# Kernel optimization log

Measured on AMD Instinct MI355X. Metric: run time of the kernel, lower is better.

Reference implementation:

```python
import jax, jax.numpy as jnp
import numpy as np

TOP_K = 2
EPS = 1e-10


def setup_inputs() -> dict:
    key = jax.random.key(0)
    k1, k2, k3, k4 = jax.random.split(key, 4)
    B, S, H, E = 4, 2048, 1024, 8
    tokens = jax.random.normal(k1, (B, S, H), dtype=jnp.float32)
    router_w = jax.random.normal(k2, (E, H), dtype=jnp.float32) * (1.0 / np.sqrt(H))
    router_b = jax.random.normal(k3, (E,), dtype=jnp.float32) * 0.01
    expert_weights = jax.random.normal(k4, (E, H, H), dtype=jnp.float32) * (1.0 / np.sqrt(H))
    return {"tokens": tokens, "router_w": router_w, "router_b": router_b,
            "expert_weights": expert_weights}


def reference(tokens, router_w, router_b, expert_weights):
    B, S, H = tokens.shape
    E = expert_weights.shape[0]
    # Router (torch Linear: x @ W^T + b)
    logits = jnp.einsum('bsh,eh->bse', tokens, router_w) + router_b  # [B,S,E]
    probs = jax.nn.softmax(logits, axis=-1)
    top_p, top_i = jax.lax.top_k(probs, TOP_K)            # [B,S,K]
    w = top_p / (jnp.sum(top_p, axis=-1, keepdims=True) + EPS)  # normalized weights

    x = tokens.reshape(-1, H)                              # [N,H]
    idx = top_i.reshape(-1, TOP_K)                         # [N,K]
    wf = w.reshape(-1, TOP_K)                              # [N,K]

    # Expert GEMM: compute all experts then gather selected (dense, vectorized
    # equivalent of the sort/pad/grouped-GEMM dispatch; padded rows with
    # original_indices==-1 never contribute to the output).
    y_all = jnp.einsum('nh,ehd->ned', x, expert_weights)   # [N,E,H]
    y_k = jnp.take_along_axis(y_all, idx[:, :, None], axis=1)  # [N,K,H]

    out = jnp.einsum('nk,nkh->nh', wf, y_k)                # weighted combine
    acc = jnp.clip(jnp.sum(wf, axis=-1), EPS, None)        # weight accumulator
    out = (out / acc[:, None]).reshape(B, S, H)

    # epsilon scale tying output to normalized router probs (gradient path)
    scale = 1.0 + jnp.sum(w, axis=-1, keepdims=True) * EPS  # [B,S,1]
    return out * scale
```

## Files before the change

kernel.cpp:

```cpp
#include <hip/hip_runtime.h>
#include <stdint.h>

#define N_TOK 8192
#define H_DIM 1024
#define N_EXP 8
#define MAX_TILES 136

typedef __bf16 bf16x8 __attribute__((ext_vector_type(8)));
typedef float floatx4 __attribute__((ext_vector_type(4)));

typedef __attribute__((address_space(1))) void GV;
typedef __attribute__((address_space(3))) void LV;

static __device__ __forceinline__ unsigned short f2b(float f) {
    union { float f; unsigned int i; } v; v.f = f;
    unsigned int u = v.i;
    return (unsigned short)((u + 0x7FFFu + ((u >> 16) & 1u)) >> 16);
}
static __device__ __forceinline__ float b2f(unsigned short u) {
    union { unsigned int i; float f; } v; v.i = ((unsigned int)u) << 16; return v.f;
}

__global__ __launch_bounds__(256) void k_front(
    const float* __restrict__ tokens,
    const float* __restrict__ router_w,
    const float* __restrict__ router_b,
    const float* __restrict__ W,
    int* __restrict__ sel, float* __restrict__ w_arr,
    unsigned short* __restrict__ tokb,
    unsigned short* __restrict__ Bp)
{
    const int t = threadIdx.x;

    if (blockIdx.x >= 2048) {
        const int idx = blockIdx.x - 2048;
        const int kg = idx & 127;
        const int e  = idx >> 7;
        const int d  = t * 4;
        const float* src = W + ((size_t)e * H_DIM + kg * 8) * H_DIM + d;
        float col[8][4];
#pragma unroll
        for (int j = 0; j < 8; ++j) {
            float4 v = *(const float4*)(src + (size_t)j * H_DIM);
            col[j][0] = v.x; col[j][1] = v.y; col[j][2] = v.z; col[j][3] = v.w;
        }
        unsigned short* dst = Bp + ((size_t)(e * 128 + kg) * H_DIM + d) * 8;
#pragma unroll
        for (int k = 0; k < 4; ++k) {
            unsigned short v[8];
#pragma unroll
            for (int j = 0; j < 8; ++j) v[j] = f2b(col[j][k]);
            *(uint4*)(dst + (size_t)k * 8) = *(uint4*)v;
        }
        return;
    }

    const int wave = t >> 6;
    const int lane = t & 63;
    const int n = blockIdx.x * 4 + wave;

    const float* xp = tokens + (size_t)n * H_DIM + lane * 16;
    float x[16];
#pragma unroll
    for (int i = 0; i < 4; ++i) {
        float4 v = *(const float4*)(xp + i * 4);
        x[i * 4 + 0] = v.x; x[i * 4 + 1] = v.y; x[i * 4 + 2] = v.z; x[i * 4 + 3] = v.w;
    }

    {
        unsigned short xb[16];
#pragma unroll
        for (int j = 0; j < 16; ++j) xb[j] = f2b(x[j]);
        unsigned short* dp = tokb + (size_t)n * H_DIM + lane * 16;
        *(uint4*)(dp)     = *(uint4*)(xb);
        *(uint4*)(dp + 8) = *(uint4*)(xb + 8);
    }

    float acc[N_EXP];
#pragma unroll
    for (int e = 0; e < N_EXP; ++e) {
        const float* wp = router_w + e * H_DIM + lane * 16;
        float s = 0.f;
#pragma unroll
        for (int i = 0; i < 4; ++i) {
            float4 v = *(const float4*)(wp + i * 4);
            s += x[i * 4 + 0] * v.x + x[i * 4 + 1] * v.y
               + x[i * 4 + 2] * v.z + x[i * 4 + 3] * v.w;
        }
        acc[e] = s;
    }

#pragma unroll
    for (int e = 0; e < N_EXP; ++e) {
        float a = acc[e];
#pragma unroll
        for (int off = 32; off > 0; off >>= 1) a += __shfl_xor(a, off);
        acc[e] = a;
    }

    if (lane == 0) {
        float lg[N_EXP];
#pragma unroll
        for (int e = 0; e < N_EXP; ++e) lg[e] = acc[e] + router_b[e];
        int e0 = 0;
#pragma unroll
        for (int e = 1; e < N_EXP; ++e) if (lg[e] > lg[e0]) e0 = e;
        int e1 = -1;
#pragma unroll
        for (int e = 0; e < N_EXP; ++e) {
            if (e == e0) continue;
            if (e1 < 0 || lg[e] > lg[e1]) e1 = e;
        }
        float w0 = 1.f / (1.f + __expf(lg[e1] - lg[e0]));
        float w1 = 1.f - w0;
        sel[n] = e0 | (e1 << 4);
        w_arr[n * 2] = w0;
        w_arr[n * 2 + 1] = w1;
    }
}

__global__ __launch_bounds__(256) void k_scan(
    const int* __restrict__ sel, int* __restrict__ cnt, int* __restrict__ bucket)
{
    __shared__ int ssel[N_TOK + N_TOK / 32];
    __shared__ int sc[256];
    const int e = blockIdx.x;
    const int t = threadIdx.x;
#pragma unroll
    for (int i = 0; i < 32; ++i) {
        int n = i * 256 + t;
        ssel[n + (n >> 5)] = sel[n];
    }
    __syncthreads();
    const int base = t * 32;
    int c = 0;
#pragma unroll
    for (int i = 0; i < 32; ++i) {
        int n = base + i;
        int s = ssel[n + (n >> 5)];
        c += ((s & 15) == e) + (((s >> 4) & 15) == e);
    }
    sc[t] = c;
    __syncthreads();
    for (int off = 1; off < 256; off <<= 1) {
        int v = (t >= off) ? sc[t - off] : 0;
        __syncthreads();
        sc[t] += v;
        __syncthreads();
    }
    int pos = sc[t] - c;
    if (t == 255) cnt[e] = sc[255];
#pragma unroll
    for (int i = 0; i < 32; ++i) {
        int n = base + i;
        int s = ssel[n + (n >> 5)];
        if ((s & 15) == e)        bucket[e * N_TOK + pos++] = 2 * n;
        if (((s >> 4) & 15) == e) bucket[e * N_TOK + pos++] = 2 * n + 1;
    }
}

__global__ __launch_bounds__(256, 4) void k_gemm(
    const unsigned short* __restrict__ tokb,
    const unsigned short* __restrict__ Bp,
    const int* __restrict__ cnt, const int* __restrict__ bucket,
    unsigned short* __restrict__ Y)
{
    const int nt = blockIdx.x & 7;
    const int tile = blockIdx.x >> 3;
    int base = 0, e = 0, mt = -1;
#pragma unroll
    for (int ee = 0; ee < 8; ++ee) {
        int te = (cnt[ee] + 127) >> 7;
        if (tile >= base && tile < base + te) { e = ee; mt = tile - base; }
        base += te;
    }
    if (mt < 0) return;
    const int cnt_local = cnt[e] - mt * 128;

    __shared__ __align__(16) unsigned short Asm[128 * 64];
    __shared__ __align__(16) unsigned short Bsm[8 * 128 * 8];
    __shared__ int rows[128];

    const int t = threadIdx.x;
    if (t < 128)
        rows[t] = (t < cnt_local) ? bucket[e * N_TOK + mt * 128 + t] : -1;
    __syncthreads();

    const int wv = t >> 6, lane = t & 63;
    const int d0 = nt * 128;

    const int p_sw = (lane & 7) ^ ((lane >> 3) & 7);
    const unsigned short* aptr[4];
#pragma unroll
    for (int i = 0; i < 4; ++i) {
        int r = i * 32 + wv * 8 + (lane >> 3);
        int rid = rows[r];
        int tok = (rid >= 0) ? (rid >> 1) : 0;
        aptr[i] = tokb + (size_t)tok * H_DIM + p_sw * 8;
    }
    const unsigned short* bbase = Bp
        + ((size_t)(e * 128 + (t >> 7)) * H_DIM + d0 + (t & 127)) * 8;

    const int w_row = wv >> 1, w_col = wv & 1;
    const int m_lane = lane & 15, quad = lane >> 4;
    const int r7 = m_lane & 7;

    floatx4 acc[4][4];
#pragma unroll
    for (int i = 0; i < 4; ++i)
#pragma unroll
        for (int j = 0; j < 4; ++j) acc[i][j] = (floatx4){0.f, 0.f, 0.f, 0.f};

    for (int kt = 0; kt < H_DIM / 64; ++kt) {
#pragma unroll
        for (int i = 0; i < 4; ++i) {
            __builtin_amdgcn_global_load_lds(
                (GV*)(aptr[i] + kt * 64),
                (LV*)(&Asm[i * 2048 + wv * 512]), 16, 0, 0);
            __builtin_amdgcn_global_load_lds(
                (GV*)(bbase + (size_t)i * 16384 + (size_t)kt * 65536),
                (LV*)(&Bsm[i * 2048 + wv * 512]), 16, 0, 0);
        }
        __syncthreads();

#pragma unroll
        for (int s = 0; s < 2; ++s) {
            bf16x8 a[4], b[4];
#pragma unroll
            for (int i = 0; i < 4; ++i) {
                int row = w_row * 64 + i * 16 + m_lane;
                a[i] = *(const bf16x8*)&Asm[row * 64 + ((s * 4 + quad) ^ r7) * 8];
            }
#pragma unroll
            for (int j = 0; j < 4; ++j)
                b[j] = *(const bf16x8*)&Bsm[((s * 4 + quad) * 128 + w_col * 64 + j * 16 + m_lane) * 8];
#pragma unroll
            for (int i = 0; i < 4; ++i)
#pragma unroll
                for (int j = 0; j < 4; ++j)
                    acc[i][j] = __builtin_amdgcn_mfma_f32_16x16x32_bf16(a[i], b[j], acc[i][j], 0, 0, 0);
        }
        __syncthreads();
    }

#pragma unroll
    for (int i = 0; i < 4; ++i) {
        const int lr_base = w_row * 64 + i * 16 + quad * 4;
#pragma unroll
        for (int reg = 0; reg < 4; ++reg) {
            const int lr = lr_base + reg;
            const int rid = rows[lr];
            if (rid >= 0) {
                unsigned short v[4];
#pragma unroll
                for (int j = 0; j < 4; ++j) v[j] = f2b(acc[i][j][reg]);
                *(uint2*)(Y + (size_t)rid * H_DIM + d0 + w_col * 64 + m_lane * 4) = *(uint2*)v;
            }
        }
    }
}

__global__ __launch_bounds__(256) void k_combine(
    const unsigned short* __restrict__ Y, const float* __restrict__ w_arr,
    float* __restrict__ out)
{
    const int g = blockIdx.x * 256 + threadIdx.x;
    const int n = g >> 7;
    const int c = (g & 127) * 8;
    const unsigned short* y0 = Y + (size_t)(2 * n) * H_DIM + c;
    const unsigned short* y1 = y0 + H_DIM;
    uint4 a = *(const uint4*)y0;
    uint4 b = *(const uint4*)y1;
    const unsigned short* pa = (const unsigned short*)&a;
    const unsigned short* pb = (const unsigned short*)&b;
    const float w0 = w_arr[2 * n], w1 = w_arr[2 * n + 1];
    const int seg = c >> 7;
    const int sl0 = c & 127;
    float* op = out + (size_t)n * H_DIM + seg * 128;
#pragma unroll
    for (int k = 0; k < 8; ++k) {
        int sl = sl0 + k;
        int wc = sl >> 6, m = (sl >> 2) & 15, j = sl & 3;
        int d = wc * 64 + j * 16 + m;
        op[d] = w0 * b2f(pa[k]) + w1 * b2f(pb[k]);
    }
}

extern "C" void kernel_launch(void* const* d_in, const int* in_sizes, int n_in,
                              void* d_out, int out_size, void* d_ws, size_t ws_size,
                              hipStream_t stream)
{
    const float* tokens   = (const float*)d_in[0];
    const float* router_w = (const float*)d_in[1];
    const float* router_b = (const float*)d_in[2];
    const float* W        = (const float*)d_in[3];
    float* out = (float*)d_out;

    char* ws = (char*)d_ws;
    int*   cnt    = (int*)(ws);
    int*   sel    = (int*)(ws + 1024);
    float* w_arr  = (float*)(ws + 34816);
    int*   bucket = (int*)(ws + 100352);
    unsigned short* tokb = (unsigned short*)(ws + 362496);
    unsigned short* Bp   = (unsigned short*)(ws + 17139712);
    unsigned short* Y    = (unsigned short*)(ws + 33916928);

    k_front  <<<2048 + 1024, 256, 0, stream>>>(tokens, router_w, router_b, W,
                                               sel, w_arr, tokb, Bp);
    k_scan   <<<N_EXP, 256, 0, stream>>>(sel, cnt, bucket);
    k_gemm   <<<MAX_TILES * 8, 256, 0, stream>>>(tokb, Bp, cnt, bucket, Y);
    k_combine<<<N_TOK * (H_DIM / 8) / 256, 256, 0, stream>>>(Y, w_arr, out);
}
```

Measured before the change: 194.8 us.

## Widen GEMM tile to 256 columns and use 1024-thread scan blocks

The grouped expert GEMM tile grows from 128x128 to 128x256 output columns per block. Each A (token) tile loaded into LDS now feeds twice as many MFMAs, halving redundant gathered-token loads, and the grid shrinks accordingly. Accumulator registers double, so launch bounds drop to 2 waves per SIMD, which lowers occupancy and latency hiding. Separately, the bucket scan kernel uses 1024 threads per expert block with 8 tokens each, shortening the serial per-thread loops at the cost of more scan steps.

```diff
diff --git a/kernel.cpp b/kernel.cpp
--- a/kernel.cpp
+++ b/kernel.cpp
@@ -119,39 +119,39 @@
     }
 }
 
-__global__ __launch_bounds__(256) void k_scan(
+__global__ __launch_bounds__(1024) void k_scan(
     const int* __restrict__ sel, int* __restrict__ cnt, int* __restrict__ bucket)
 {
     __shared__ int ssel[N_TOK + N_TOK / 32];
-    __shared__ int sc[256];
+    __shared__ int sc[1024];
     const int e = blockIdx.x;
     const int t = threadIdx.x;
 #pragma unroll
-    for (int i = 0; i < 32; ++i) {
-        int n = i * 256 + t;
+    for (int i = 0; i < 8; ++i) {
+        int n = i * 1024 + t;
         ssel[n + (n >> 5)] = sel[n];
     }
     __syncthreads();
-    const int base = t * 32;
+    const int base = t * 8;
     int c = 0;
 #pragma unroll
-    for (int i = 0; i < 32; ++i) {
+    for (int i = 0; i < 8; ++i) {
         int n = base + i;
         int s = ssel[n + (n >> 5)];
         c += ((s & 15) == e) + (((s >> 4) & 15) == e);
     }
     sc[t] = c;
     __syncthreads();
-    for (int off = 1; off < 256; off <<= 1) {
+    for (int off = 1; off < 1024; off <<= 1) {
         int v = (t >= off) ? sc[t - off] : 0;
         __syncthreads();
         sc[t] += v;
         __syncthreads();
     }
     int pos = sc[t] - c;
-    if (t == 255) cnt[e] = sc[255];
-#pragma unroll
-    for (int i = 0; i < 32; ++i) {
+    if (t == 1023) cnt[e] = sc[1023];
+#pragma unroll
+    for (int i = 0; i < 8; ++i) {
         int n = base + i;
         int s = ssel[n + (n >> 5)];
         if ((s & 15) == e)        bucket[e * N_TOK + pos++] = 2 * n;
@@ -159,14 +159,14 @@
     }
 }
 
-__global__ __launch_bounds__(256, 4) void k_gemm(
+__global__ __launch_bounds__(256, 2) void k_gemm(
     const unsigned short* __restrict__ tokb,
     const unsigned short* __restrict__ Bp,
     const int* __restrict__ cnt, const int* __restrict__ bucket,
     unsigned short* __restrict__ Y)
 {
-    const int nt = blockIdx.x & 7;
-    const int tile = blockIdx.x >> 3;
+    const int ntp = blockIdx.x & 3;
+    const int tile = blockIdx.x >> 2;
     int base = 0, e = 0, mt = -1;
 #pragma unroll
     for (int ee = 0; ee < 8; ++ee) {
@@ -178,7 +178,7 @@
     const int cnt_local = cnt[e] - mt * 128;
 
     __shared__ __align__(16) unsigned short Asm[128 * 64];
-    __shared__ __align__(16) unsigned short Bsm[8 * 128 * 8];
+    __shared__ __align__(16) unsigned short Bsm[2 * 8 * 128 * 8];
     __shared__ int rows[128];
 
     const int t = threadIdx.x;
@@ -187,7 +187,7 @@
     __syncthreads();
 
     const int wv = t >> 6, lane = t & 63;
-    const int d0 = nt * 128;
+    const int d0 = ntp * 256;
 
     const int p_sw = (lane & 7) ^ ((lane >> 3) & 7);
     const unsigned short* aptr[4];
@@ -198,47 +198,60 @@
         int tok = (rid >= 0) ? (rid >> 1) : 0;
         aptr[i] = tokb + (size_t)tok * H_DIM + p_sw * 8;
     }
-    const unsigned short* bbase = Bp
-        + ((size_t)(e * 128 + (t >> 7)) * H_DIM + d0 + (t & 127)) * 8;
+    const unsigned short* bbase[2];
+#pragma unroll
+    for (int seg = 0; seg < 2; ++seg)
+        bbase[seg] = Bp + ((size_t)(e * 128 + (t >> 7)) * H_DIM + d0 + seg * 128 + (t & 127)) * 8;
 
     const int w_row = wv >> 1, w_col = wv & 1;
     const int m_lane = lane & 15, quad = lane >> 4;
     const int r7 = m_lane & 7;
 
-    floatx4 acc[4][4];
+    floatx4 acc[4][2][4];
 #pragma unroll
     for (int i = 0; i < 4; ++i)
 #pragma unroll
-        for (int j = 0; j < 4; ++j) acc[i][j] = (floatx4){0.f, 0.f, 0.f, 0.f};
+        for (int seg = 0; seg < 2; ++seg)
+#pragma unroll
+            for (int j = 0; j < 4; ++j) acc[i][seg][j] = (floatx4){0.f, 0.f, 0.f, 0.f};
 
     for (int kt = 0; kt < H_DIM / 64; ++kt) {
 #pragma unroll
-        for (int i = 0; i < 4; ++i) {
+        for (int i = 0; i < 4; ++i)
             __builtin_amdgcn_global_load_lds(
                 (GV*)(aptr[i] + kt * 64),
                 (LV*)(&Asm[i * 2048 + wv * 512]), 16, 0, 0);
-            __builtin_amdgcn_global_load_lds(
-                (GV*)(bbase + (size_t)i * 16384 + (size_t)kt * 65536),
-                (LV*)(&Bsm[i * 2048 + wv * 512]), 16, 0, 0);
-        }
+#pragma unroll
+        for (int seg = 0; seg < 2; ++seg)
+#pragma unroll
+            for (int i = 0; i < 4; ++i)
+                __builtin_amdgcn_global_load_lds(
+                    (GV*)(bbase[seg] + (size_t)i * 16384 + (size_t)kt * 65536),
+                    (LV*)(&Bsm[seg * 8192 + i * 2048 + wv * 512]), 16, 0, 0);
         __syncthreads();
 
 #pragma unroll
         for (int s = 0; s < 2; ++s) {
-            bf16x8 a[4], b[4];
+            bf16x8 a[4], b[2][4];
 #pragma unroll
             for (int i = 0; i < 4; ++i) {
                 int row = w_row * 64 + i * 16 + m_lane;
                 a[i] = *(const bf16x8*)&Asm[row * 64 + ((s * 4 + quad) ^ r7) * 8];
             }
 #pragma unroll
-            for (int j = 0; j < 4; ++j)
-                b[j] = *(const bf16x8*)&Bsm[((s * 4 + quad) * 128 + w_col * 64 + j * 16 + m_lane) * 8];
+            for (int seg = 0; seg < 2; ++seg)
+#pragma unroll
+                for (int j = 0; j < 4; ++j)
+                    b[seg][j] = *(const bf16x8*)&Bsm[seg * 8192
+                        + ((s * 4 + quad) * 128 + w_col * 64 + j * 16 + m_lane) * 8];
 #pragma unroll
             for (int i = 0; i < 4; ++i)
 #pragma unroll
-                for (int j = 0; j < 4; ++j)
-                    acc[i][j] = __builtin_amdgcn_mfma_f32_16x16x32_bf16(a[i], b[j], acc[i][j], 0, 0, 0);
+                for (int seg = 0; seg < 2; ++seg)
+#pragma unroll
+                    for (int j = 0; j < 4; ++j)
+                        acc[i][seg][j] = __builtin_amdgcn_mfma_f32_16x16x32_bf16(
+                            a[i], b[seg][j], acc[i][seg][j], 0, 0, 0);
         }
         __syncthreads();
     }
@@ -251,10 +264,14 @@
             const int lr = lr_base + reg;
             const int rid = rows[lr];
             if (rid >= 0) {
-                unsigned short v[4];
-#pragma unroll
-                for (int j = 0; j < 4; ++j) v[j] = f2b(acc[i][j][reg]);
-                *(uint2*)(Y + (size_t)rid * H_DIM + d0 + w_col * 64 + m_lane * 4) = *(uint2*)v;
+#pragma unroll
+                for (int seg = 0; seg < 2; ++seg) {
+                    unsigned short v[4];
+#pragma unroll
+                    for (int j = 0; j < 4; ++j) v[j] = f2b(acc[i][seg][j][reg]);
+                    *(uint2*)(Y + (size_t)rid * H_DIM + d0 + seg * 128
+                              + w_col * 64 + m_lane * 4) = *(uint2*)v;
+                }
             }
         }
     }
@@ -307,7 +324,7 @@
 
     k_front  <<<2048 + 1024, 256, 0, stream>>>(tokens, router_w, router_b, W,
                                                sel, w_arr, tokb, Bp);
-    k_scan   <<<N_EXP, 256, 0, stream>>>(sel, cnt, bucket);
-    k_gemm   <<<MAX_TILES * 8, 256, 0, stream>>>(tokb, Bp, cnt, bucket, Y);
+    k_scan   <<<N_EXP, 1024, 0, stream>>>(sel, cnt, bucket);
+    k_gemm   <<<MAX_TILES * 4, 256, 0, stream>>>(tokb, Bp, cnt, bucket, Y);
     k_combine<<<N_TOK * (H_DIM / 8) / 256, 256, 0, stream>>>(Y, w_arr, out);
 }
```

Result: no change. 195.2 us (+0.2%).

## Double-buffer GEMM LDS tiles with async prefetch and widen scan to 1024 threads

Applied to the files above, without the earlier changes.

The expert GEMM now keeps two LDS buffers for A and B and issues the global-to-LDS loads for the next k-tile before computing on the current one. It waits with a partial vmcnt and raw s_barrier, so memory latency can overlap MFMA work. LDS use doubles and the launch-bounds occupancy hint drops from 4 to 2 blocks per CU. Separately, the scan kernel uses 1024 threads per expert with 8 elements each instead of 256 with 32, which shortens its serial per-thread loops but lengthens the prefix-sum barrier chain.

```diff
diff --git a/kernel.cpp b/kernel.cpp
--- a/kernel.cpp
+++ b/kernel.cpp
@@ -119,39 +119,39 @@
     }
 }
 
-__global__ __launch_bounds__(256) void k_scan(
+__global__ __launch_bounds__(1024) void k_scan(
     const int* __restrict__ sel, int* __restrict__ cnt, int* __restrict__ bucket)
 {
     __shared__ int ssel[N_TOK + N_TOK / 32];
-    __shared__ int sc[256];
+    __shared__ int sc[1024];
     const int e = blockIdx.x;
     const int t = threadIdx.x;
 #pragma unroll
-    for (int i = 0; i < 32; ++i) {
-        int n = i * 256 + t;
+    for (int i = 0; i < 8; ++i) {
+        int n = i * 1024 + t;
         ssel[n + (n >> 5)] = sel[n];
     }
     __syncthreads();
-    const int base = t * 32;
+    const int base = t * 8;
     int c = 0;
 #pragma unroll
-    for (int i = 0; i < 32; ++i) {
+    for (int i = 0; i < 8; ++i) {
         int n = base + i;
         int s = ssel[n + (n >> 5)];
         c += ((s & 15) == e) + (((s >> 4) & 15) == e);
     }
     sc[t] = c;
     __syncthreads();
-    for (int off = 1; off < 256; off <<= 1) {
+    for (int off = 1; off < 1024; off <<= 1) {
         int v = (t >= off) ? sc[t - off] : 0;
         __syncthreads();
         sc[t] += v;
         __syncthreads();
     }
     int pos = sc[t] - c;
-    if (t == 255) cnt[e] = sc[255];
-#pragma unroll
-    for (int i = 0; i < 32; ++i) {
+    if (t == 1023) cnt[e] = sc[1023];
+#pragma unroll
+    for (int i = 0; i < 8; ++i) {
         int n = base + i;
         int s = ssel[n + (n >> 5)];
         if ((s & 15) == e)        bucket[e * N_TOK + pos++] = 2 * n;
@@ -159,7 +159,7 @@
     }
 }
 
-__global__ __launch_bounds__(256, 4) void k_gemm(
+__global__ __launch_bounds__(256, 2) void k_gemm(
     const unsigned short* __restrict__ tokb,
     const unsigned short* __restrict__ Bp,
     const int* __restrict__ cnt, const int* __restrict__ bucket,
@@ -177,8 +177,8 @@
     if (mt < 0) return;
     const int cnt_local = cnt[e] - mt * 128;
 
-    __shared__ __align__(16) unsigned short Asm[128 * 64];
-    __shared__ __align__(16) unsigned short Bsm[8 * 128 * 8];
+    __shared__ __align__(16) unsigned short Asm[2][128 * 64];
+    __shared__ __align__(16) unsigned short Bsm[2][8 * 128 * 8];
     __shared__ int rows[128];
 
     const int t = threadIdx.x;
@@ -204,6 +204,7 @@
     const int w_row = wv >> 1, w_col = wv & 1;
     const int m_lane = lane & 15, quad = lane >> 4;
     const int r7 = m_lane & 7;
+    const int lds_off = wv * 512;
 
     floatx4 acc[4][4];
 #pragma unroll
@@ -211,36 +212,53 @@
 #pragma unroll
         for (int j = 0; j < 4; ++j) acc[i][j] = (floatx4){0.f, 0.f, 0.f, 0.f};
 
-    for (int kt = 0; kt < H_DIM / 64; ++kt) {
-#pragma unroll
-        for (int i = 0; i < 4; ++i) {
-            __builtin_amdgcn_global_load_lds(
-                (GV*)(aptr[i] + kt * 64),
-                (LV*)(&Asm[i * 2048 + wv * 512]), 16, 0, 0);
-            __builtin_amdgcn_global_load_lds(
-                (GV*)(bbase + (size_t)i * 16384 + (size_t)kt * 65536),
-                (LV*)(&Bsm[i * 2048 + wv * 512]), 16, 0, 0);
-        }
-        __syncthreads();
-
+#pragma unroll
+    for (int i = 0; i < 4; ++i)
+        __builtin_amdgcn_global_load_lds((GV*)(aptr[i]),
+            (LV*)(&Asm[0][i * 2048 + lds_off]), 16, 0, 0);
+#pragma unroll
+    for (int i = 0; i < 4; ++i)
+        __builtin_amdgcn_global_load_lds((GV*)(bbase + (size_t)i * 16384),
+            (LV*)(&Bsm[0][i * 2048 + lds_off]), 16, 0, 0);
+
+    for (int kt = 0; kt < 16; ++kt) {
+        const int cur = kt & 1, nxt = cur ^ 1;
+        if (kt < 15) {
+#pragma unroll
+            for (int i = 0; i < 4; ++i)
+                __builtin_amdgcn_global_load_lds((GV*)(aptr[i] + (kt + 1) * 64),
+                    (LV*)(&Asm[nxt][i * 2048 + lds_off]), 16, 0, 0);
+#pragma unroll
+            for (int i = 0; i < 4; ++i)
+                __builtin_amdgcn_global_load_lds(
+                    (GV*)(bbase + (size_t)i * 16384 + (size_t)(kt + 1) * 65536),
+                    (LV*)(&Bsm[nxt][i * 2048 + lds_off]), 16, 0, 0);
+            asm volatile("s_waitcnt vmcnt(8)" ::: "memory");
+        } else {
+            asm volatile("s_waitcnt vmcnt(0)" ::: "memory");
+        }
+        asm volatile("s_barrier" ::: "memory");
+
+        const unsigned short* As_c = &Asm[cur][0];
+        const unsigned short* Bs_c = &Bsm[cur][0];
 #pragma unroll
         for (int s = 0; s < 2; ++s) {
             bf16x8 a[4], b[4];
 #pragma unroll
             for (int i = 0; i < 4; ++i) {
                 int row = w_row * 64 + i * 16 + m_lane;
-                a[i] = *(const bf16x8*)&Asm[row * 64 + ((s * 4 + quad) ^ r7) * 8];
+                a[i] = *(const bf16x8*)&As_c[row * 64 + ((s * 4 + quad) ^ r7) * 8];
             }
 #pragma unroll
             for (int j = 0; j < 4; ++j)
-                b[j] = *(const bf16x8*)&Bsm[((s * 4 + quad) * 128 + w_col * 64 + j * 16 + m_lane) * 8];
+                b[j] = *(const bf16x8*)&Bs_c[((s * 4 + quad) * 128 + w_col * 64 + j * 16 + m_lane) * 8];
 #pragma unroll
             for (int i = 0; i < 4; ++i)
 #pragma unroll
                 for (int j = 0; j < 4; ++j)
                     acc[i][j] = __builtin_amdgcn_mfma_f32_16x16x32_bf16(a[i], b[j], acc[i][j], 0, 0, 0);
         }
-        __syncthreads();
+        asm volatile("s_barrier" ::: "memory");
     }
 
 #pragma unroll
@@ -307,7 +325,7 @@
 
     k_front  <<<2048 + 1024, 256, 0, stream>>>(tokens, router_w, router_b, W,
                                                sel, w_arr, tokb, Bp);
-    k_scan   <<<N_EXP, 256, 0, stream>>>(sel, cnt, bucket);
+    k_scan   <<<N_EXP, 1024, 0, stream>>>(sel, cnt, bucket);
     k_gemm   <<<MAX_TILES * 8, 256, 0, stream>>>(tokb, Bp, cnt, bucket, Y);
     k_combine<<<N_TOK * (H_DIM / 8) / 256, 256, 0, stream>>>(Y, w_arr, out);
 }
```

Result: slower. 199.7 us (+2.5%).
